# Kernel optimization log

Hardware: AMD Instinct MI355X
Metric: run time of the kernel (lower is better)

## Reference

```python
import jax, jax.numpy as jnp
import numpy as np

D_MODEL = 1024
NUM_EXPERTS = 64
TOP_K = 2
TEMPERATURE = 1.0


def setup_inputs() -> dict:
    key = jax.random.key(0)
    k1, k2, k3, k4 = jax.random.split(key, 4)
    mh_output = jax.random.normal(k1, (8, 4096, D_MODEL), dtype=jnp.float32)
    noise = jax.random.normal(k2, (8, 4096, NUM_EXPERTS), dtype=jnp.float32)  # randn_like sample, externalized
    # nn.Linear weights: shape [out, in], init normal(0, 0.02); biases zero
    W_route = jax.random.normal(k3, (NUM_EXPERTS, D_MODEL), dtype=jnp.float32) * 0.02
    b_route = jnp.zeros((NUM_EXPERTS,), dtype=jnp.float32)
    W_noise = jax.random.normal(k4, (NUM_EXPERTS, D_MODEL), dtype=jnp.float32) * 0.02
    b_noise = jnp.zeros((NUM_EXPERTS,), dtype=jnp.float32)
    return {"mh_output": mh_output, "noise": noise, "W_route": W_route,
            "b_route": b_route, "W_noise": W_noise, "b_noise": b_noise}


def reference(mh_output, noise, W_route, b_route, W_noise, b_noise):
    # logits = topkroute_linear(mh_output); noise_logits = noise_linear(mh_output)
    logits = jnp.einsum('bsd,ed->bse', mh_output, W_route) + b_route
    noise_logits = jnp.einsum('bsd,ed->bse', mh_output, W_noise) + b_noise
    # noisy logits = logits + temperature * randn * softplus(noise_logits)
    noisy = logits + TEMPERATURE * noise * jax.nn.softplus(noise_logits)
    # top-k, scatter into -inf, softmax  ==  softmax over top-k values scattered into zeros
    top_vals, indices = jax.lax.top_k(noisy, TOP_K)          # [b, s, k]
    probs_k = jax.nn.softmax(top_vals, axis=-1)              # softmax(-inf elsewhere) -> 0 elsewhere
    one_hot = jax.nn.one_hot(indices, NUM_EXPERTS, dtype=noisy.dtype)  # [b, s, k, E]
    router_output = jnp.sum(one_hot * probs_k[..., None], axis=-2)     # [b, s, E]
    return router_output, indices
```

## Files before the change

### kernel.cpp

```cpp
#include <hip/hip_runtime.h>
#include <hip/hip_bf16.h>
#include <math.h>


#define T_TOKENS 32768
#define D_MODEL  1024
#define NE       64
#define NCOL     128
#define M_TILE   64
#define NCHUNK   32
#define CS_LD    68
#define OUT_IDX_BASE ((size_t)T_TOKENS * NE)
#define W_ELEMS  (NCOL * D_MODEL)

typedef short  bf16x8  __attribute__((ext_vector_type(8)));
typedef float  floatx4 __attribute__((ext_vector_type(4)));

__device__ __forceinline__ float softplus_f(float x) {
    return fmaxf(x, 0.f) + log1pf(expf(-fabsf(x)));
}

__device__ __forceinline__ void cvt8frag(const float4 a, const float4 b,
                                         bf16x8* hi, bf16x8* lo) {
    float v[8] = {a.x, a.y, a.z, a.w, b.x, b.y, b.z, b.w};
    int hw[4], lw[4];
    #pragma unroll
    for (int p = 0; p < 4; ++p) {
        float2 f2 = make_float2(v[2 * p], v[2 * p + 1]);
        __hip_bfloat162 h2 = __float22bfloat162_rn(f2);
        int u; __builtin_memcpy(&u, &h2, 4);
        float h0 = __uint_as_float(((unsigned)u) << 16);
        float h1 = __uint_as_float(((unsigned)u) & 0xFFFF0000u);
        float2 l2 = make_float2(v[2 * p] - h0, v[2 * p + 1] - h1);
        __hip_bfloat162 L2 = __float22bfloat162_rn(l2);
        int ul; __builtin_memcpy(&ul, &L2, 4);
        hw[p] = u; lw[p] = ul;
    }
    int4 hp = make_int4(hw[0], hw[1], hw[2], hw[3]);
    int4 lp = make_int4(lw[0], lw[1], lw[2], lw[3]);
    __builtin_memcpy(hi, &hp, 16);
    __builtin_memcpy(lo, &lp, 16);
}

__global__ __launch_bounds__(256) void prepack_w(
    const float* __restrict__ Wr, const float* __restrict__ Wn,
    short* __restrict__ Bh, short* __restrict__ Bl)
{
    int g   = blockIdx.x * 256 + threadIdx.x;
    int n   = g & 15;
    int kg  = (g >> 4) & 127;
    int t2  = g >> 11;
    int col = t2 * 16 + n;
    const float* src = (col < NE ? Wr + (size_t)col * D_MODEL
                                 : Wn + (size_t)(col - NE) * D_MODEL) + kg * 8;
    float4 a = *(const float4*)src;
    float4 b = *(const float4*)(src + 4);
    bf16x8 hi, lo;
    cvt8frag(a, b, &hi, &lo);
    *(bf16x8*)(Bh + (size_t)g * 8) = hi;
    *(bf16x8*)(Bl + (size_t)g * 8) = lo;
}

__global__ __launch_bounds__(256) void router_mfma(
    const float* __restrict__ A,
    const float* __restrict__ noise,
    const float* __restrict__ br,
    const float* __restrict__ bn,
    const short* __restrict__ Bh,
    const short* __restrict__ Bl,
    float* __restrict__ out)
{
    __shared__ float Cs[M_TILE * CS_LD];
    __shared__ float s_p1[M_TILE], s_p2[M_TILE];
    __shared__ int   s_e1[M_TILE], s_e2[M_TILE];

    const int tid  = threadIdx.x;
    const int lane = tid & 63;
    const int wid  = tid >> 6;
    const int th   = wid >> 1;
    const int wc   = wid & 1;
    const int n16  = lane & 15;
    const int quad = lane >> 4;
    const int m0   = blockIdx.x * M_TILE;

    const float* pA0 = A + (size_t)(m0 + th * 32 + n16) * D_MODEL + quad * 8;
    const float* pA1 = pA0 + (size_t)16 * D_MODEL;

    int bBase[4];
    #pragma unroll
    for (int f = 0; f < 4; ++f) {
        int ntile = (f < 2) ? (wc * 2 + f) : (4 + wc * 2 + (f - 2));
        bBase[f] = ((ntile * 128 + quad) * 16 + n16) * 8;
    }

    floatx4 acc[2][4];
    #pragma unroll
    for (int mf = 0; mf < 2; ++mf)
        #pragma unroll
        for (int f = 0; f < 4; ++f) acc[mf][f] = (floatx4)0.f;

    float4 r1[2][2], r2[2][2];
    bf16x8 ah[2], al[2];
    {
        float4 r0a0 = *(const float4*)(pA0);
        float4 r0a1 = *(const float4*)(pA0 + 4);
        float4 r0b0 = *(const float4*)(pA1);
        float4 r0b1 = *(const float4*)(pA1 + 4);
        r1[0][0] = *(const float4*)(pA0 + 32);  r1[0][1] = *(const float4*)(pA0 + 36);
        r1[1][0] = *(const float4*)(pA1 + 32);  r1[1][1] = *(const float4*)(pA1 + 36);
        r2[0][0] = *(const float4*)(pA0 + 64);  r2[0][1] = *(const float4*)(pA0 + 68);
        r2[1][0] = *(const float4*)(pA1 + 64);  r2[1][1] = *(const float4*)(pA1 + 68);
        cvt8frag(r0a0, r0a1, &ah[0], &al[0]);
        cvt8frag(r0b0, r0b1, &ah[1], &al[1]);
    }
    bf16x8 bhc[4], blc[4];
    #pragma unroll
    for (int f = 0; f < 4; ++f) {
        bhc[f] = *(const bf16x8*)(Bh + bBase[f]);
        blc[f] = *(const bf16x8*)(Bl + bBase[f]);
    }

    for (int kc = 0; kc < NCHUNK; ++kc) {
        float4 r3[2][2];
        if (kc + 3 < NCHUNK) {
            const int o = (kc + 3) * 32;
            r3[0][0] = *(const float4*)(pA0 + o);  r3[0][1] = *(const float4*)(pA0 + o + 4);
            r3[1][0] = *(const float4*)(pA1 + o);  r3[1][1] = *(const float4*)(pA1 + o + 4);
        }
        bf16x8 bhn[4], bln[4];
        if (kc + 1 < NCHUNK) {
            const int o = (kc + 1) * 512;
            #pragma unroll
            for (int f = 0; f < 4; ++f) {
                bhn[f] = *(const bf16x8*)(Bh + bBase[f] + o);
                bln[f] = *(const bf16x8*)(Bl + bBase[f] + o);
            }
        }

        #pragma unroll
        for (int mf = 0; mf < 2; ++mf)
            #pragma unroll
            for (int f = 0; f < 4; ++f) {
                acc[mf][f] = __builtin_amdgcn_mfma_f32_16x16x32_bf16(ah[mf], bhc[f], acc[mf][f], 0, 0, 0);
                acc[mf][f] = __builtin_amdgcn_mfma_f32_16x16x32_bf16(ah[mf], blc[f], acc[mf][f], 0, 0, 0);
                acc[mf][f] = __builtin_amdgcn_mfma_f32_16x16x32_bf16(al[mf], bhc[f], acc[mf][f], 0, 0, 0);
            }

        if (kc + 1 < NCHUNK) {
            cvt8frag(r1[0][0], r1[0][1], &ah[0], &al[0]);
            cvt8frag(r1[1][0], r1[1][1], &ah[1], &al[1]);
        }

        #pragma unroll
        for (int mf = 0; mf < 2; ++mf) {
            r1[mf][0] = r2[mf][0]; r1[mf][1] = r2[mf][1];
            r2[mf][0] = r3[mf][0]; r2[mf][1] = r3[mf][1];
        }
        #pragma unroll
        for (int f = 0; f < 4; ++f) { bhc[f] = bhn[f]; blc[f] = bln[f]; }
    }

    #pragma unroll
    for (int fi = 0; fi < 2; ++fi) {
        int e = wc * 32 + fi * 16 + n16;
        float brv = br[e], bnv = bn[e];
        #pragma unroll
        for (int mf = 0; mf < 2; ++mf)
            #pragma unroll
            for (int rr = 0; rr < 4; ++rr) {
                int t = th * 32 + mf * 16 + quad * 4 + rr;
                float nz    = noise[(size_t)(m0 + t) * NE + e];
                float route = acc[mf][fi]     [rr] + brv;
                float nl    = acc[mf][fi + 2] [rr] + bnv;
                Cs[t * CS_LD + e] = fmaf(nz, softplus_f(nl), route);
            }
    }
    __syncthreads();

    if (tid < M_TILE) {
        const int t = tid;
        float v1 = -INFINITY, v2 = -INFINITY;
        int e1 = 0, e2 = 0;
        #pragma unroll
        for (int e4 = 0; e4 < 16; ++e4) {
            float4 q = *(const float4*)&Cs[t * CS_LD + e4 * 4];
            float qa[4] = {q.x, q.y, q.z, q.w};
            #pragma unroll
            for (int c = 0; c < 4; ++c) {
                float v = qa[c];
                int e = e4 * 4 + c;
                if (v > v1) { v2 = v1; e2 = e1; v1 = v; e1 = e; }
                else if (v > v2) { v2 = v; e2 = e; }
            }
        }
        float ex = expf(v2 - v1);
        float denom = 1.f + ex;
        s_p1[t] = 1.f / denom;
        s_p2[t] = ex / denom;
        s_e1[t] = e1;
        s_e2[t] = e2;
        float2 iv = make_float2((float)e1, (float)e2);
        *(float2*)(out + OUT_IDX_BASE + (size_t)(m0 + t) * 2) = iv;
    }
    __syncthreads();

    #pragma unroll
    for (int i = 0; i < 4; ++i) {
        int gi = i * 256 + tid;
        int t  = gi >> 4;
        int e0 = (gi & 15) * 4;
        float p1 = s_p1[t], p2 = s_p2[t];
        int   e1 = s_e1[t], e2 = s_e2[t];
        float4 v;
        v.x = (e0 + 0 == e1) ? p1 : ((e0 + 0 == e2) ? p2 : 0.f);
        v.y = (e0 + 1 == e1) ? p1 : ((e0 + 1 == e2) ? p2 : 0.f);
        v.z = (e0 + 2 == e1) ? p1 : ((e0 + 2 == e2) ? p2 : 0.f);
        v.w = (e0 + 3 == e1) ? p1 : ((e0 + 3 == e2) ? p2 : 0.f);
        *(float4*)(out + (size_t)(m0 + t) * NE + e0) = v;
    }
}

extern "C" void kernel_launch(void* const* d_in, const int* in_sizes, int n_in,
                              void* d_out, int out_size, void* d_ws, size_t ws_size,
                              hipStream_t stream) {
    const float* A     = (const float*)d_in[0];
    const float* noise = (const float*)d_in[1];
    const float* Wr    = (const float*)d_in[2];
    const float* br    = (const float*)d_in[3];
    const float* Wn    = (const float*)d_in[4];
    const float* bn    = (const float*)d_in[5];
    float* out = (float*)d_out;

    short* Bh = (short*)d_ws;
    short* Bl = Bh + W_ELEMS;

    prepack_w<<<dim3(W_ELEMS / 8 / 256), dim3(256), 0, stream>>>(Wr, Wn, Bh, Bl);
    router_mfma<<<dim3(T_TOKENS / M_TILE), dim3(256), 0, stream>>>(A, noise, br, bn, Bh, Bl, out);
}
```

Before: 243.6 us.

## Stage A tiles via global_load_lds double buffer with smaller token tiles

```diff
diff --git a/kernel.cpp b/kernel.cpp
--- a/kernel.cpp
+++ b/kernel.cpp
@@ -7,7 +7,7 @@
 #define D_MODEL  1024
 #define NE       64
 #define NCOL     128
-#define M_TILE   64
+#define M_TILE   32
 #define NCHUNK   32
 #define CS_LD    68
 #define OUT_IDX_BASE ((size_t)T_TOKENS * NE)
@@ -18,6 +18,12 @@
 
 __device__ __forceinline__ float softplus_f(float x) {
     return fmaxf(x, 0.f) + log1pf(expf(-fabsf(x)));
+}
+
+__device__ __forceinline__ void gload_lds16(const float* g, void* l) {
+    __builtin_amdgcn_global_load_lds(
+        (const __attribute__((address_space(1))) void*)g,
+        (__attribute__((address_space(3))) void*)l, 16, 0, 0);
 }
 
 __device__ __forceinline__ void cvt8frag(const float4 a, const float4 b,
@@ -61,7 +67,7 @@
     *(bf16x8*)(Bl + (size_t)g * 8) = lo;
 }
 
-__global__ __launch_bounds__(256) void router_mfma(
+__global__ __launch_bounds__(256, 4) void router_mfma(
     const float* __restrict__ A,
     const float* __restrict__ noise,
     const float* __restrict__ br,
@@ -70,6 +76,7 @@
     const short* __restrict__ Bl,
     float* __restrict__ out)
 {
+    __shared__ __align__(16) float Abuf[2][M_TILE * 32];
     __shared__ float Cs[M_TILE * CS_LD];
     __shared__ float s_p1[M_TILE], s_p2[M_TILE];
     __shared__ int   s_e1[M_TILE], s_e2[M_TILE];
@@ -77,101 +84,80 @@
     const int tid  = threadIdx.x;
     const int lane = tid & 63;
     const int wid  = tid >> 6;
-    const int th   = wid >> 1;
-    const int wc   = wid & 1;
     const int n16  = lane & 15;
     const int quad = lane >> 4;
     const int m0   = blockIdx.x * M_TILE;
 
-    const float* pA0 = A + (size_t)(m0 + th * 32 + n16) * D_MODEL + quad * 8;
-    const float* pA1 = pA0 + (size_t)16 * D_MODEL;
-
-    int bBase[4];
-    #pragma unroll
-    for (int f = 0; f < 4; ++f) {
-        int ntile = (f < 2) ? (wc * 2 + f) : (4 + wc * 2 + (f - 2));
-        bBase[f] = ((ntile * 128 + quad) * 16 + n16) * 8;
-    }
-
-    floatx4 acc[2][4];
-    #pragma unroll
-    for (int mf = 0; mf < 2; ++mf)
-        #pragma unroll
-        for (int f = 0; f < 4; ++f) acc[mf][f] = (floatx4)0.f;
-
-    float4 r1[2][2], r2[2][2];
-    bf16x8 ah[2], al[2];
+    const int srow = (wid << 3) + (lane >> 3);
+    const int schk = (lane & 7) ^ (lane >> 3);
+    const float* gA = A + (size_t)(m0 + srow) * D_MODEL + schk * 4;
+    float* lb0 = &Abuf[0][wid * 256];
+    float* lb1 = &Abuf[1][wid * 256];
+
+    const int bBaseR = ((wid * 128 + quad) * 16 + n16) * 8;
+    const int bBaseN = (((wid + 4) * 128 + quad) * 16 + n16) * 8;
+
+    int rdOff[2][2];
+    #pragma unroll
+    for (int mf = 0; mf < 2; ++mf) {
+        int r  = mf * 16 + n16;
+        int s0 = (2 * quad)     ^ (n16 & 7);
+        int s1 = (2 * quad + 1) ^ (n16 & 7);
+        rdOff[mf][0] = r * 32 + s0 * 4;
+        rdOff[mf][1] = r * 32 + s1 * 4;
+    }
+
+    floatx4 accR[2], accN[2];
+    #pragma unroll
+    for (int mf = 0; mf < 2; ++mf) { accR[mf] = (floatx4)0.f; accN[mf] = (floatx4)0.f; }
+
+    gload_lds16(gA, lb0);
+    __syncthreads();
+
+    for (int kc = 0; kc < NCHUNK; ++kc) {
+        const int cur = kc & 1;
+
+        if (kc + 1 < NCHUNK)
+            gload_lds16(gA + (kc + 1) * 32, (cur ? lb0 : lb1));
+
+        const int o = kc * 512;
+        bf16x8 bhR = *(const bf16x8*)(Bh + bBaseR + o);
+        bf16x8 blR = *(const bf16x8*)(Bl + bBaseR + o);
+        bf16x8 bhN = *(const bf16x8*)(Bh + bBaseN + o);
+        bf16x8 blN = *(const bf16x8*)(Bl + bBaseN + o);
+
+        bf16x8 ah[2], al[2];
+        #pragma unroll
+        for (int mf = 0; mf < 2; ++mf) {
+            float4 f0 = *(const float4*)&Abuf[cur][rdOff[mf][0]];
+            float4 f1 = *(const float4*)&Abuf[cur][rdOff[mf][1]];
+            cvt8frag(f0, f1, &ah[mf], &al[mf]);
+        }
+
+        #pragma unroll
+        for (int mf = 0; mf < 2; ++mf) {
+            accR[mf] = __builtin_amdgcn_mfma_f32_16x16x32_bf16(ah[mf], bhR, accR[mf], 0, 0, 0);
+            accR[mf] = __builtin_amdgcn_mfma_f32_16x16x32_bf16(ah[mf], blR, accR[mf], 0, 0, 0);
+            accR[mf] = __builtin_amdgcn_mfma_f32_16x16x32_bf16(al[mf], bhR, accR[mf], 0, 0, 0);
+            accN[mf] = __builtin_amdgcn_mfma_f32_16x16x32_bf16(ah[mf], bhN, accN[mf], 0, 0, 0);
+            accN[mf] = __builtin_amdgcn_mfma_f32_16x16x32_bf16(ah[mf], blN, accN[mf], 0, 0, 0);
+            accN[mf] = __builtin_amdgcn_mfma_f32_16x16x32_bf16(al[mf], bhN, accN[mf], 0, 0, 0);
+        }
+
+        __syncthreads();
+    }
+
     {
-        float4 r0a0 = *(const float4*)(pA0);
-        float4 r0a1 = *(const float4*)(pA0 + 4);
-        float4 r0b0 = *(const float4*)(pA1);
-        float4 r0b1 = *(const float4*)(pA1 + 4);
-        r1[0][0] = *(const float4*)(pA0 + 32);  r1[0][1] = *(const float4*)(pA0 + 36);
-        r1[1][0] = *(const float4*)(pA1 + 32);  r1[1][1] = *(const float4*)(pA1 + 36);
-        r2[0][0] = *(const float4*)(pA0 + 64);  r2[0][1] = *(const float4*)(pA0 + 68);
-        r2[1][0] = *(const float4*)(pA1 + 64);  r2[1][1] = *(const float4*)(pA1 + 68);
-        cvt8frag(r0a0, r0a1, &ah[0], &al[0]);
-        cvt8frag(r0b0, r0b1, &ah[1], &al[1]);
-    }
-    bf16x8 bhc[4], blc[4];
-    #pragma unroll
-    for (int f = 0; f < 4; ++f) {
-        bhc[f] = *(const bf16x8*)(Bh + bBase[f]);
-        blc[f] = *(const bf16x8*)(Bl + bBase[f]);
-    }
-
-    for (int kc = 0; kc < NCHUNK; ++kc) {
-        float4 r3[2][2];
-        if (kc + 3 < NCHUNK) {
-            const int o = (kc + 3) * 32;
-            r3[0][0] = *(const float4*)(pA0 + o);  r3[0][1] = *(const float4*)(pA0 + o + 4);
-            r3[1][0] = *(const float4*)(pA1 + o);  r3[1][1] = *(const float4*)(pA1 + o + 4);
-        }
-        bf16x8 bhn[4], bln[4];
-        if (kc + 1 < NCHUNK) {
-            const int o = (kc + 1) * 512;
-            #pragma unroll
-            for (int f = 0; f < 4; ++f) {
-                bhn[f] = *(const bf16x8*)(Bh + bBase[f] + o);
-                bln[f] = *(const bf16x8*)(Bl + bBase[f] + o);
-            }
-        }
-
-        #pragma unroll
-        for (int mf = 0; mf < 2; ++mf)
-            #pragma unroll
-            for (int f = 0; f < 4; ++f) {
-                acc[mf][f] = __builtin_amdgcn_mfma_f32_16x16x32_bf16(ah[mf], bhc[f], acc[mf][f], 0, 0, 0);
-                acc[mf][f] = __builtin_amdgcn_mfma_f32_16x16x32_bf16(ah[mf], blc[f], acc[mf][f], 0, 0, 0);
-                acc[mf][f] = __builtin_amdgcn_mfma_f32_16x16x32_bf16(al[mf], bhc[f], acc[mf][f], 0, 0, 0);
-            }
-
-        if (kc + 1 < NCHUNK) {
-            cvt8frag(r1[0][0], r1[0][1], &ah[0], &al[0]);
-            cvt8frag(r1[1][0], r1[1][1], &ah[1], &al[1]);
-        }
-
-        #pragma unroll
-        for (int mf = 0; mf < 2; ++mf) {
-            r1[mf][0] = r2[mf][0]; r1[mf][1] = r2[mf][1];
-            r2[mf][0] = r3[mf][0]; r2[mf][1] = r3[mf][1];
-        }
-        #pragma unroll
-        for (int f = 0; f < 4; ++f) { bhc[f] = bhn[f]; blc[f] = bln[f]; }
-    }
-
-    #pragma unroll
-    for (int fi = 0; fi < 2; ++fi) {
-        int e = wc * 32 + fi * 16 + n16;
+        int e = wid * 16 + n16;
         float brv = br[e], bnv = bn[e];
         #pragma unroll
         for (int mf = 0; mf < 2; ++mf)
             #pragma unroll
             for (int rr = 0; rr < 4; ++rr) {
-                int t = th * 32 + mf * 16 + quad * 4 + rr;
+                int t = mf * 16 + quad * 4 + rr;
                 float nz    = noise[(size_t)(m0 + t) * NE + e];
-                float route = acc[mf][fi]     [rr] + brv;
-                float nl    = acc[mf][fi + 2] [rr] + bnv;
+                float route = accR[mf][rr] + brv;
+                float nl    = accN[mf][rr] + bnv;
                 Cs[t * CS_LD + e] = fmaf(nz, softplus_f(nl), route);
             }
     }
@@ -205,7 +191,7 @@
     __syncthreads();
 
     #pragma unroll
-    for (int i = 0; i < 4; ++i) {
+    for (int i = 0; i < 2; ++i) {
         int gi = i * 256 + tid;
         int t  = gi >> 4;
         int e0 = (gi & 15) * 4;
```

New measurement: 234.2 us. 3.9% less time.
